# Performance work log

Measured on AMD Instinct MI355X. Metric: run time of the kernel, lower is better.

The kernel has to match this reference:

```python
import jax, jax.numpy as jnp
import numpy as np

H = 64
N_BENE, N_DIAG, N_TREAT = 200000, 10000, 100000
E = 1000000
N_INST = 500000

def setup_inputs() -> dict:
    key = jax.random.key(0)
    ks = jax.random.split(key, 24)
    def lin(k, din, dout):
        kw, kb = jax.random.split(k)
        s = 1.0 / np.sqrt(din)
        return (jax.random.uniform(kw, (din, dout), jnp.float32, -s, s),
                jax.random.uniform(kb, (dout,), jnp.float32, -s, s))
    inp = {
        'bene_ids': jax.random.randint(ks[0], (N_BENE,), 0, 10000, jnp.int32),
        'diag_ids': jax.random.randint(ks[1], (N_DIAG,), 0, 200, jnp.int32),
        'treatment_ids': jax.random.randint(ks[2], (N_TREAT,), 0, 1000, jnp.int32),
        'b2d_src': jax.random.randint(ks[3], (E,), 0, N_BENE, jnp.int32),
        'b2d_dst': jax.random.randint(ks[4], (E,), 0, N_DIAG, jnp.int32),
        't2d_src': jax.random.randint(ks[5], (E,), 0, N_TREAT, jnp.int32),
        't2d_dst': jax.random.randint(ks[6], (E,), 0, N_DIAG, jnp.int32),
        'inst2type': jax.random.randint(ks[7], (N_INST,), 0, N_DIAG, jnp.int32),
        'bene_emb': jax.random.normal(ks[8], (10000, H), jnp.float32),
        'diag_emb': jax.random.normal(ks[9], (200, H), jnp.float32),
        'treat_emb': jax.random.normal(ks[10], (1000, H), jnp.float32),
    }
    # two conv layers: msg_bene_to_diag (Wb,bb), msg_treatment_to_diag (Wt,bt), update_diag (Wu,bu)
    names = ['Wb0','bb0','Wt0','bt0','Wu0','bu0','Wb1','bb1','Wt1','bt1','Wu1','bu1']
    idx = 11
    for i in range(0, len(names), 2):
        W, b = lin(ks[idx], H, H); idx += 1
        inp[names[i]] = W; inp[names[i+1]] = b
    inp['oW1'], inp['ob1'] = lin(ks[idx], H, H // 2); idx += 1
    inp['oW2'], inp['ob2'] = lin(ks[idx], H // 2, 1)
    return inp

def _conv(bene, diag, treat, b2d_src, b2d_dst, t2d_src, t2d_dst, Wb, bb, Wt, bt, Wu, bu):
    msg_b = bene[b2d_src] @ Wb + bb                      # [E, H]
    agg_b = jax.ops.segment_sum(msg_b, b2d_dst, num_segments=N_DIAG)
    msg_t = treat[t2d_src] @ Wt + bt                     # [E, H]
    agg_t = jax.ops.segment_sum(msg_t, t2d_dst, num_segments=N_DIAG)
    combined = 0.5 * (agg_b + agg_t)                     # mean over 2 message types
    return combined @ Wu + bu

def reference(bene_ids, diag_ids, treatment_ids, b2d_src, b2d_dst, t2d_src, t2d_dst,
              inst2type, bene_emb, diag_emb, treat_emb,
              Wb0, bb0, Wt0, bt0, Wu0, bu0, Wb1, bb1, Wt1, bt1, Wu1, bu1,
              oW1, ob1, oW2, ob2):
    bene = bene_emb[bene_ids]
    diag = diag_emb[diag_ids]
    treat = treat_emb[treatment_ids]
    for (Wb, bb, Wt, bt, Wu, bu) in ((Wb0, bb0, Wt0, bt0, Wu0, bu0),
                                     (Wb1, bb1, Wt1, bt1, Wu1, bu1)):
        diag = _conv(bene, diag, treat, b2d_src, b2d_dst, t2d_src, t2d_dst,
                     Wb, bb, Wt, bt, Wu, bu)
        bene, diag, treat = jax.nn.relu(bene), jax.nn.relu(diag), jax.nn.relu(treat)
    inst = diag[inst2type]                               # [N_INST, H]
    h = jax.nn.relu(inst @ oW1 + ob1)                    # dropout is eval-mode identity
    return jax.nn.sigmoid(h @ oW2 + ob2)[:, 0]
```

## Files before the change

kernel.cpp:

```cpp
#include <hip/hip_runtime.h>
#include <hip/hip_bf16.h>

#define Hdim 64
#define NDIAG 10000
#define NEDGE 1000000
#define NINST 500000
#define NBENE_EMB 10000
#define NTREAT_EMB 1000

#define NSUP 79
#define SSHIFT 7
#define SMASK 127
#define CAP_S 13568
#define BUFK 64
#define EPB 2048
#define NSPB 489
#define NSPLIT 4
#define FPSCALE 1048576.0f
#define FPINV (1.0f / 1048576.0f)

__global__ __launch_bounds__(512) void prep_kernel(
    const float* __restrict__ bene_emb, const float* __restrict__ treat_emb,
    int* __restrict__ itab_b, int* __restrict__ itab_t, int* __restrict__ gcur_all) {
    int gid = blockIdx.x * 512 + threadIdx.x;
    if (gid < 2 * NSUP) gcur_all[gid] = 0;
    if (gid < NBENE_EMB * Hdim) {
        itab_b[gid] = (int)(fmaxf(bene_emb[gid], 0.f) * FPSCALE);
    } else {
        int g2 = gid - NBENE_EMB * Hdim;
        if (g2 < NTREAT_EMB * Hdim)
            itab_t[g2] = (int)(fmaxf(treat_emb[g2], 0.f) * FPSCALE);
    }
}

__global__ __launch_bounds__(512) void split_kernel(
    const int* __restrict__ b2d_dst, const int* __restrict__ b2d_src, const int* __restrict__ bene_ids,
    const int* __restrict__ t2d_dst, const int* __restrict__ t2d_src, const int* __restrict__ treat_ids,
    int* __restrict__ gcur_b, int* __restrict__ gbuf_b,
    int* __restrict__ gcur_t, int* __restrict__ gbuf_t) {
    const int ty = blockIdx.y;
    const int* dst  = ty ? t2d_dst  : b2d_dst;
    const int* src  = ty ? t2d_src  : b2d_src;
    const int* ids  = ty ? treat_ids: bene_ids;
    int* gcur = ty ? gcur_t : gcur_b;
    int* gbuf = ty ? gbuf_t : gbuf_b;

    __shared__ int buf[NSUP][BUFK];
    __shared__ int cnt[NSUP];
    __shared__ int base_s[NSUP];
    const int tid = threadIdx.x;
    for (int i = tid; i < NSUP; i += 512) cnt[i] = 0;
    __syncthreads();

    const int e4 = blockIdx.x * EPB + tid * 4;
    if (e4 < NEDGE) {
        int4 d4 = *reinterpret_cast<const int4*>(dst + e4);
        int4 s4 = *reinterpret_cast<const int4*>(src + e4);
        int dd[4] = {d4.x, d4.y, d4.z, d4.w};
        int ss[4] = {s4.x, s4.y, s4.z, s4.w};
        int cc[4];
        #pragma unroll
        for (int u = 0; u < 4; ++u) cc[u] = ids[ss[u]];
        #pragma unroll
        for (int u = 0; u < 4; ++u) {
            int b = dd[u] >> SSHIFT;
            int v = ((dd[u] & SMASK) << 16) | cc[u];
            int p = atomicAdd(&cnt[b], 1);
            if (p < BUFK) {
                buf[b][p] = v;
            } else {
                int gp = atomicAdd(&gcur[b], 1);
                if (gp < CAP_S) gbuf[b * CAP_S + gp] = v;
            }
        }
    }
    __syncthreads();

    const int wid = tid >> 6, lane = tid & 63;
    if (wid < 2) {
        int b = (wid << 6) + lane;
        if (b < NSUP) {
            int n = min(cnt[b], BUFK);
            base_s[b] = atomicAdd(&gcur[b], n);
        }
    }
    __syncthreads();

    for (int b = wid; b < NSUP; b += 8) {
        int n = min(cnt[b], BUFK);
        int gp0 = base_s[b];
        for (int k = lane; k < n; k += 64) {
            int gp = gp0 + k;
            if (gp < CAP_S) gbuf[b * CAP_S + gp] = buf[b][k];
        }
    }
}

__global__ __launch_bounds__(512) void agg_kernel(
    const int* __restrict__ gbuf_b, const int* __restrict__ gcur_b, const int* __restrict__ itab_b,
    const int* __restrict__ gbuf_t, const int* __restrict__ gcur_t, const int* __restrict__ itab_t,
    int* __restrict__ pbuf, int* __restrict__ pbufd) {
    const int bk = blockIdx.x, ty = blockIdx.y, sp = blockIdx.z;
    const int* gbuf = ty ? gbuf_t : gbuf_b;
    const int* gcur = ty ? gcur_t : gcur_b;
    const int* itab = ty ? itab_t : itab_b;

    __shared__ int acc[128][64];
    __shared__ int dhist[128];

    const int tid = threadIdx.x;
    const int wid = tid >> 6, lane = tid & 63;
    int4* a4 = (int4*)&acc[0][0];
    for (int i = tid; i < 2048; i += 512) a4[i] = int4{0, 0, 0, 0};
    if (tid < 128) dhist[tid] = 0;
    __syncthreads();

    const int count = min(gcur[bk], CAP_S);
    const int slice = (count + NSPLIT - 1) / NSPLIT;
    const int s0 = sp * slice;
    const int s1 = min(count, s0 + slice);
    const int n = max(0, s1 - s0);
    const int nfull = n >> 6;
    const int rem = n & 63;
    const int* bucket = gbuf + bk * CAP_S;

    for (int ck = wid; ck < nfull; ck += 8) {
        int vv = bucket[s0 + (ck << 6) + lane];
        atomicAdd(&dhist[(vv >> 16) & SMASK], 1);
        #pragma unroll
        for (int g = 0; g < 8; ++g) {
            int dla[8], iv[8];
            #pragma unroll
            for (int u = 0; u < 8; ++u) {
                int s = __builtin_amdgcn_readlane(vv, g * 8 + u);
                dla[u] = (s >> 16) & SMASK;
                iv[u] = itab[(s & 0xffff) * Hdim + lane];
            }
            #pragma unroll
            for (int u = 0; u < 8; ++u)
                atomicAdd(&acc[dla[u]][lane], iv[u]);
        }
    }
    if (rem && wid == (nfull & 7)) {
        int base2 = s0 + (nfull << 6);
        int vv = (lane < rem) ? bucket[base2 + lane] : 0;
        if (lane < rem) atomicAdd(&dhist[(vv >> 16) & SMASK], 1);
        for (int u = 0; u < rem; ++u) {
            int s = __builtin_amdgcn_readlane(vv, u);
            atomicAdd(&acc[(s >> 16) & SMASK][lane], itab[(s & 0xffff) * Hdim + lane]);
        }
    }
    __syncthreads();

    int4* o4 = (int4*)(pbuf + (size_t)((ty * NSUP + bk) * NSPLIT + sp) * 8192);
    for (int i = tid; i < 2048; i += 512) o4[i] = a4[i];
    if (tid < 128)
        pbufd[(size_t)((ty * NSUP + bk) * NSPLIT + sp) * 128 + tid] = dhist[tid];
}

__global__ __launch_bounds__(256) void head_kernel(
    const int* __restrict__ pbuf, const int* __restrict__ pbufd,
    const float* __restrict__ Wb1, const float* __restrict__ bb1,
    const float* __restrict__ Wt1, const float* __restrict__ bt1,
    const float* __restrict__ Wu1, const float* __restrict__ bu1,
    const float* __restrict__ oW1, const float* __restrict__ ob1,
    const float* __restrict__ oW2, const float* __restrict__ ob2,
    float* __restrict__ per_diag_out) {
    int wave = threadIdx.x >> 6;
    int lane = threadIdx.x & 63;
    int d = blockIdx.x * 4 + wave;

    __shared__ float Sb[4][64];
    __shared__ float St[4][64];
    __shared__ float Cc[4][64];
    __shared__ float Dd[4][64];

    const int bk = d >> SSHIFT, row = d & SMASK;
    const int* pb = pbuf + (size_t)(bk * NSPLIT) * 8192;
    const int* pt = pbuf + (size_t)((NSUP + bk) * NSPLIT) * 8192;
    int sbi = 0, sti = 0, dgb = 0, dgt = 0;
    #pragma unroll
    for (int sp = 0; sp < NSPLIT; ++sp) {
        sbi += pb[sp * 8192 + row * 64 + lane];
        sti += pt[sp * 8192 + row * 64 + lane];
        dgb += pbufd[(size_t)(bk * NSPLIT + sp) * 128 + row];
        dgt += pbufd[(size_t)((NSUP + bk) * NSPLIT + sp) * 128 + row];
    }
    Sb[wave][lane] = (float)sbi * FPINV;
    St[wave][lane] = (float)sti * FPINV;
    __syncthreads();

    float ab = (float)dgb * bb1[lane];
    float at = (float)dgt * bt1[lane];
    #pragma unroll 8
    for (int l = 0; l < Hdim; ++l) {
        ab += Sb[wave][l] * Wb1[l * Hdim + lane];
        at += St[wave][l] * Wt1[l * Hdim + lane];
    }
    float comb = 0.5f * (ab + at);
    Cc[wave][lane] = comb;
    __syncthreads();

    float dg = bu1[lane];
    #pragma unroll 8
    for (int l = 0; l < Hdim; ++l) dg += Cc[wave][l] * Wu1[l * Hdim + lane];
    float d1 = fmaxf(dg, 0.f);
    Dd[wave][lane] = d1;
    __syncthreads();

    float contrib = 0.f;
    if (lane < 32) {
        float h = ob1[lane];
        #pragma unroll 8
        for (int l = 0; l < Hdim; ++l) h += Dd[wave][l] * oW1[l * 32 + lane];
        h = fmaxf(h, 0.f);
        contrib = h * oW2[lane];
    }
    for (int o = 32; o > 0; o >>= 1) contrib += __shfl_down(contrib, o);
    if (lane == 0) {
        float logit = contrib + ob2[0];
        per_diag_out[d] = 1.f / (1.f + __expf(-logit));
    }
}

__global__ void gather_kernel(const int* __restrict__ inst2type,
                              const float* __restrict__ per_diag_out,
                              float* __restrict__ out) {
    int i = blockIdx.x * blockDim.x + threadIdx.x;
    int i4 = i * 4;
    if (i4 >= NINST) return;
    int4 t = *reinterpret_cast<const int4*>(inst2type + i4);
    float4 r;
    r.x = per_diag_out[t.x];
    r.y = per_diag_out[t.y];
    r.z = per_diag_out[t.z];
    r.w = per_diag_out[t.w];
    *reinterpret_cast<float4*>(out + i4) = r;
}

extern "C" void kernel_launch(void* const* d_in, const int* in_sizes, int n_in,
                              void* d_out, int out_size, void* d_ws, size_t ws_size,
                              hipStream_t stream) {
    (void)in_sizes; (void)n_in; (void)out_size; (void)ws_size;

    const int*   bene_ids  = (const int*)d_in[0];
    const int*   treat_ids = (const int*)d_in[2];
    const int*   b2d_src   = (const int*)d_in[3];
    const int*   b2d_dst   = (const int*)d_in[4];
    const int*   t2d_src   = (const int*)d_in[5];
    const int*   t2d_dst   = (const int*)d_in[6];
    const int*   inst2type = (const int*)d_in[7];
    const float* bene_emb  = (const float*)d_in[8];
    const float* treat_emb = (const float*)d_in[10];
    const float* Wb1 = (const float*)d_in[17];
    const float* bb1 = (const float*)d_in[18];
    const float* Wt1 = (const float*)d_in[19];
    const float* bt1 = (const float*)d_in[20];
    const float* Wu1 = (const float*)d_in[21];
    const float* bu1 = (const float*)d_in[22];
    const float* oW1 = (const float*)d_in[23];
    const float* ob1 = (const float*)d_in[24];
    const float* oW2 = (const float*)d_in[25];
    const float* ob2 = (const float*)d_in[26];
    float* out = (float*)d_out;

    char* w = (char*)d_ws;
    auto alloc = [&](size_t bytes) {
        char* p = w;
        w += (bytes + 255) & ~(size_t)255;
        return p;
    };
    int* gcur_all = (int*)alloc(2 * NSUP * 4);
    int* gcur_b = gcur_all;
    int* gcur_t = gcur_all + NSUP;
    int* gbuf_b = (int*)alloc((size_t)NSUP * CAP_S * 4);
    int* gbuf_t = (int*)alloc((size_t)NSUP * CAP_S * 4);
    int* itab_b = (int*)alloc((size_t)NBENE_EMB * Hdim * 4);
    int* itab_t = (int*)alloc((size_t)NTREAT_EMB * Hdim * 4);
    int* pbuf   = (int*)alloc((size_t)2 * NSUP * NSPLIT * 8192 * 4);
    int* pbufd  = (int*)alloc((size_t)2 * NSUP * NSPLIT * 128 * 4);
    float* pdo  = (float*)alloc(NDIAG * 4);

    prep_kernel<<<(NBENE_EMB + NTREAT_EMB) * Hdim / 512, 512, 0, stream>>>(
        bene_emb, treat_emb, itab_b, itab_t, gcur_all);

    split_kernel<<<dim3(NSPB, 2), 512, 0, stream>>>(
        b2d_dst, b2d_src, bene_ids, t2d_dst, t2d_src, treat_ids,
        gcur_b, gbuf_b, gcur_t, gbuf_t);

    agg_kernel<<<dim3(NSUP, 2, NSPLIT), 512, 0, stream>>>(
        gbuf_b, gcur_b, itab_b, gbuf_t, gcur_t, itab_t, pbuf, pbufd);

    head_kernel<<<NDIAG / 4, 256, 0, stream>>>(
        pbuf, pbufd,
        Wb1, bb1, Wt1, bt1, Wu1, bu1, oW1, ob1, oW2, ob2, pdo);

    gather_kernel<<<(NINST / 4 + 255) / 256, 256, 0, stream>>>(inst2type, pdo, out);
}
```

Baseline: 213.1 us.

## Fuse prep into split kernel and reduce partial sums with global atomics

Folds the embedding-to-fixed-point prep into the split kernel as a third grid row, which also zeroes new global accumulators. The bucket-counter zeroing becomes a memset. Aggregation blocks now add their shared-memory partials directly into a single global int accumulator with atomics, replacing per-split partial buffers that the head kernel had to sum. The split count doubles from 4 to 8 for more parallelism, and the split staging buffer is transposed to change shared-memory access patterns. This trades head-kernel reads and one launch for global atomic traffic and a race between prep and split blocks inside one kernel, which is safe only because split does not read itab.

```diff
diff --git a/kernel.cpp b/kernel.cpp
--- a/kernel.cpp
+++ b/kernel.cpp
@@ -11,44 +11,49 @@
 #define NSUP 79
 #define SSHIFT 7
 #define SMASK 127
+#define NROWS (NSUP * 128)
 #define CAP_S 13568
 #define BUFK 64
 #define EPB 2048
 #define NSPB 489
-#define NSPLIT 4
+#define NSPLIT 8
 #define FPSCALE 1048576.0f
 #define FPINV (1.0f / 1048576.0f)
 
-__global__ __launch_bounds__(512) void prep_kernel(
-    const float* __restrict__ bene_emb, const float* __restrict__ treat_emb,
-    int* __restrict__ itab_b, int* __restrict__ itab_t, int* __restrict__ gcur_all) {
-    int gid = blockIdx.x * 512 + threadIdx.x;
-    if (gid < 2 * NSUP) gcur_all[gid] = 0;
-    if (gid < NBENE_EMB * Hdim) {
-        itab_b[gid] = (int)(fmaxf(bene_emb[gid], 0.f) * FPSCALE);
-    } else {
-        int g2 = gid - NBENE_EMB * Hdim;
-        if (g2 < NTREAT_EMB * Hdim)
-            itab_t[g2] = (int)(fmaxf(treat_emb[g2], 0.f) * FPSCALE);
-    }
-}
-
-__global__ __launch_bounds__(512) void split_kernel(
+__global__ __launch_bounds__(512) void split_prep_kernel(
     const int* __restrict__ b2d_dst, const int* __restrict__ b2d_src, const int* __restrict__ bene_ids,
     const int* __restrict__ t2d_dst, const int* __restrict__ t2d_src, const int* __restrict__ treat_ids,
+    const float* __restrict__ bene_emb, const float* __restrict__ treat_emb,
+    int* __restrict__ itab_b, int* __restrict__ itab_t,
     int* __restrict__ gcur_b, int* __restrict__ gbuf_b,
-    int* __restrict__ gcur_t, int* __restrict__ gbuf_t) {
+    int* __restrict__ gcur_t, int* __restrict__ gbuf_t,
+    int* __restrict__ iacc, int* __restrict__ degs) {
     const int ty = blockIdx.y;
+    const int tid = threadIdx.x;
+
+    if (ty == 2) {
+        int gid = blockIdx.x * 512 + tid;
+        const int gstride = NSPB * 512;
+        int4 z4 = {0, 0, 0, 0};
+        int4* i4 = (int4*)iacc;
+        for (int i = gid; i < 2 * NROWS * 16; i += gstride) i4[i] = z4;
+        for (int i = gid; i < 2 * NROWS; i += gstride) degs[i] = 0;
+        for (int i = gid; i < NBENE_EMB * Hdim; i += gstride)
+            itab_b[i] = (int)(fmaxf(bene_emb[i], 0.f) * FPSCALE);
+        for (int i = gid; i < NTREAT_EMB * Hdim; i += gstride)
+            itab_t[i] = (int)(fmaxf(treat_emb[i], 0.f) * FPSCALE);
+        return;
+    }
+
     const int* dst  = ty ? t2d_dst  : b2d_dst;
     const int* src  = ty ? t2d_src  : b2d_src;
     const int* ids  = ty ? treat_ids: bene_ids;
     int* gcur = ty ? gcur_t : gcur_b;
     int* gbuf = ty ? gbuf_t : gbuf_b;
 
-    __shared__ int buf[NSUP][BUFK];
+    __shared__ int buf[BUFK][NSUP];
     __shared__ int cnt[NSUP];
     __shared__ int base_s[NSUP];
-    const int tid = threadIdx.x;
     for (int i = tid; i < NSUP; i += 512) cnt[i] = 0;
     __syncthreads();
 
@@ -67,7 +72,7 @@
             int v = ((dd[u] & SMASK) << 16) | cc[u];
             int p = atomicAdd(&cnt[b], 1);
             if (p < BUFK) {
-                buf[b][p] = v;
+                buf[p][b] = v;
             } else {
                 int gp = atomicAdd(&gcur[b], 1);
                 if (gp < CAP_S) gbuf[b * CAP_S + gp] = v;
@@ -89,9 +94,9 @@
     for (int b = wid; b < NSUP; b += 8) {
         int n = min(cnt[b], BUFK);
         int gp0 = base_s[b];
-        for (int k = lane; k < n; k += 64) {
-            int gp = gp0 + k;
-            if (gp < CAP_S) gbuf[b * CAP_S + gp] = buf[b][k];
+        if (lane < n) {
+            int gp = gp0 + lane;
+            if (gp < CAP_S) gbuf[b * CAP_S + gp] = buf[lane][b];
         }
     }
 }
@@ -99,11 +104,13 @@
 __global__ __launch_bounds__(512) void agg_kernel(
     const int* __restrict__ gbuf_b, const int* __restrict__ gcur_b, const int* __restrict__ itab_b,
     const int* __restrict__ gbuf_t, const int* __restrict__ gcur_t, const int* __restrict__ itab_t,
-    int* __restrict__ pbuf, int* __restrict__ pbufd) {
+    int* __restrict__ iacc, int* __restrict__ degs) {
     const int bk = blockIdx.x, ty = blockIdx.y, sp = blockIdx.z;
     const int* gbuf = ty ? gbuf_t : gbuf_b;
     const int* gcur = ty ? gcur_t : gcur_b;
     const int* itab = ty ? itab_t : itab_b;
+    int* iac = iacc + (size_t)ty * NROWS * Hdim;
+    int* dg  = degs + ty * NROWS;
 
     __shared__ int acc[128][64];
     __shared__ int dhist[128];
@@ -152,14 +159,16 @@
     }
     __syncthreads();
 
-    int4* o4 = (int4*)(pbuf + (size_t)((ty * NSUP + bk) * NSPLIT + sp) * 8192);
-    for (int i = tid; i < 2048; i += 512) o4[i] = a4[i];
-    if (tid < 128)
-        pbufd[(size_t)((ty * NSUP + bk) * NSPLIT + sp) * 128 + tid] = dhist[tid];
+    for (int i = wid; i < 128; i += 8)
+        atomicAdd(&iac[(size_t)((bk << 7) + i) * Hdim + lane], acc[i][lane]);
+    if (tid < 128) {
+        int t = dhist[tid];
+        if (t) atomicAdd(&dg[(bk << 7) + tid], t);
+    }
 }
 
 __global__ __launch_bounds__(256) void head_kernel(
-    const int* __restrict__ pbuf, const int* __restrict__ pbufd,
+    const int* __restrict__ iacc, const int* __restrict__ degs,
     const float* __restrict__ Wb1, const float* __restrict__ bb1,
     const float* __restrict__ Wt1, const float* __restrict__ bt1,
     const float* __restrict__ Wu1, const float* __restrict__ bu1,
@@ -175,17 +184,10 @@
     __shared__ float Cc[4][64];
     __shared__ float Dd[4][64];
 
-    const int bk = d >> SSHIFT, row = d & SMASK;
-    const int* pb = pbuf + (size_t)(bk * NSPLIT) * 8192;
-    const int* pt = pbuf + (size_t)((NSUP + bk) * NSPLIT) * 8192;
-    int sbi = 0, sti = 0, dgb = 0, dgt = 0;
-    #pragma unroll
-    for (int sp = 0; sp < NSPLIT; ++sp) {
-        sbi += pb[sp * 8192 + row * 64 + lane];
-        sti += pt[sp * 8192 + row * 64 + lane];
-        dgb += pbufd[(size_t)(bk * NSPLIT + sp) * 128 + row];
-        dgt += pbufd[(size_t)((NSUP + bk) * NSPLIT + sp) * 128 + row];
-    }
+    int sbi = iacc[(size_t)d * Hdim + lane];
+    int sti = iacc[(size_t)(NROWS + d) * Hdim + lane];
+    int dgb = degs[d];
+    int dgt = degs[NROWS + d];
     Sb[wave][lane] = (float)sbi * FPINV;
     St[wave][lane] = (float)sti * FPINV;
     __syncthreads();
@@ -277,22 +279,22 @@
     int* gbuf_t = (int*)alloc((size_t)NSUP * CAP_S * 4);
     int* itab_b = (int*)alloc((size_t)NBENE_EMB * Hdim * 4);
     int* itab_t = (int*)alloc((size_t)NTREAT_EMB * Hdim * 4);
-    int* pbuf   = (int*)alloc((size_t)2 * NSUP * NSPLIT * 8192 * 4);
-    int* pbufd  = (int*)alloc((size_t)2 * NSUP * NSPLIT * 128 * 4);
+    int* iacc   = (int*)alloc((size_t)2 * NROWS * Hdim * 4);
+    int* degs   = (int*)alloc((size_t)2 * NROWS * 4);
     float* pdo  = (float*)alloc(NDIAG * 4);
 
-    prep_kernel<<<(NBENE_EMB + NTREAT_EMB) * Hdim / 512, 512, 0, stream>>>(
-        bene_emb, treat_emb, itab_b, itab_t, gcur_all);
-
-    split_kernel<<<dim3(NSPB, 2), 512, 0, stream>>>(
+    hipMemsetAsync(gcur_all, 0, 2 * NSUP * 4, stream);
+
+    split_prep_kernel<<<dim3(NSPB, 3), 512, 0, stream>>>(
         b2d_dst, b2d_src, bene_ids, t2d_dst, t2d_src, treat_ids,
-        gcur_b, gbuf_b, gcur_t, gbuf_t);
+        bene_emb, treat_emb, itab_b, itab_t,
+        gcur_b, gbuf_b, gcur_t, gbuf_t, iacc, degs);
 
     agg_kernel<<<dim3(NSUP, 2, NSPLIT), 512, 0, stream>>>(
-        gbuf_b, gcur_b, itab_b, gbuf_t, gcur_t, itab_t, pbuf, pbufd);
+        gbuf_b, gcur_b, itab_b, gbuf_t, gcur_t, itab_t, iacc, degs);
 
     head_kernel<<<NDIAG / 4, 256, 0, stream>>>(
-        pbuf, pbufd,
+        iacc, degs,
         Wb1, bb1, Wt1, bt1, Wu1, bu1, oW1, ob1, oW2, ob2, pdo);
 
     gather_kernel<<<(NINST / 4 + 255) / 256, 256, 0, stream>>>(inst2type, pdo, out);
```

After: 215.8 us. Within noise of the previous version (+1.3%).
